# Optimization experiments

Hardware: AMD Instinct MI355X
Metric: run time of the kernel (lower is better)

The kernel has to match this reference:

```python
import jax, jax.numpy as jnp
import numpy as np

C = 256      # channel_num
K = 9        # key_num
B, H, W = 8, 64, 64


def setup_inputs() -> dict:
    key = jax.random.key(0)
    ks = jax.random.split(key, 12)
    s = 1.0 / np.sqrt(C)
    return {
        "query_layer": jax.random.normal(ks[0], (B, C, H, W), jnp.float32),
        "key_layer": jax.random.normal(ks[1], (B, C, H, W), jnp.float32),
        "gumbel_noise": jax.random.gumbel(ks[2], (B, K, H, W), jnp.float32),
        "w_refer": jax.random.normal(ks[3], (C, C), jnp.float32) * s,
        "b_refer": jax.random.normal(ks[4], (C,), jnp.float32) * 0.01,
        "w_attn": jax.random.normal(ks[5], (K, C), jnp.float32) * s,
        "b_attn": jax.random.normal(ks[6], (K,), jnp.float32) * 0.01,
        "w_mask": jax.random.normal(ks[7], (K, C), jnp.float32) * s,
        "b_mask": jax.random.normal(ks[8], (K,), jnp.float32) * 0.01,
        "w_off": jax.random.normal(ks[9], (2 * K, C), jnp.float32) * 0.02,
        "b_off": jax.random.normal(ks[10], (2 * K,), jnp.float32) * 0.01,
        "temp": 1,
    }


def _conv1x1(w, b, x):
    # w: (O,C), x: (B,C,H,W) -> (B,O,H,W)
    return jnp.einsum('oc,bchw->bohw', w, x) + b[None, :, None, None]


def _sample_one(img, py, px):
    # img: (C,H,W); py,px: (K,H,W) absolute sampling coords (bilinear, zero pad)
    h, w = img.shape[1], img.shape[2]
    y0 = jnp.floor(py)
    x0 = jnp.floor(px)
    wy = py - y0          # weight toward y0+1
    wx = px - x0

    def gather(yi, xi):
        valid = (yi >= 0) & (yi < h) & (xi >= 0) & (xi < w)
        yc = jnp.clip(yi, 0, h - 1).astype(jnp.int32)
        xc = jnp.clip(xi, 0, w - 1).astype(jnp.int32)
        return img[:, yc, xc] * valid[None].astype(img.dtype)  # (C,K,H,W)

    out = (gather(y0, x0) * ((1 - wy) * (1 - wx))[None]
           + gather(y0, x0 + 1) * ((1 - wy) * wx)[None]
           + gather(y0 + 1, x0) * (wy * (1 - wx))[None]
           + gather(y0 + 1, x0 + 1) * (wy * wx)[None])
    return out  # (C,K,H,W)


def reference(query_layer, key_layer, gumbel_noise, w_refer, b_refer,
              w_attn, b_attn, w_mask, b_mask, w_off, b_off, temp):
    key_feature = _conv1x1(w_refer, b_refer, key_layer)          # (B,C,H,W)
    attn_weights = _conv1x1(w_attn, b_attn, query_layer)         # (B,K,H,W)
    soft_mask = _conv1x1(w_mask, b_mask, query_layer)            # (B,K,H,W)
    # gumbel_softmax(hard=False) over key dim
    hard_mask = jax.nn.softmax((soft_mask + gumbel_noise) / temp, axis=1)
    offset = _conv1x1(w_off, b_off, query_layer)                 # (B,2K,H,W)

    # faithful to offset[:, i:i+2]: overlapping (dy,dx) slices
    dy = offset[:, 0:K]        # (B,K,H,W)
    dx = offset[:, 1:K + 1]    # (B,K,H,W)
    ys = jnp.arange(H, dtype=offset.dtype)[None, None, :, None]
    xs = jnp.arange(W, dtype=offset.dtype)[None, None, None, :]
    py = ys + dy
    px = xs + dx

    sampled = jax.vmap(_sample_one)(key_feature, py, px)         # (B,C,K,H,W)

    aw = jax.nn.softmax(attn_weights * hard_mask, axis=1)        # (B,K,H,W)
    out = jnp.einsum('bkhw,bckhw->bchw', aw, sampled)            # (B,C,H,W)
    return out
```

## Files before the change

### kernel.cpp

```cpp
#include <hip/hip_runtime.h>

typedef unsigned short u16;
typedef __attribute__((ext_vector_type(8))) short bf16x8;
typedef __attribute__((ext_vector_type(4))) float f32x4;

__device__ __forceinline__ u16 f2bf(float f) {
    unsigned u = __float_as_uint(f);
    unsigned r = (u + 0x7fffu + ((u >> 16) & 1u)) >> 16;
    return (u16)r;
}
__device__ __forceinline__ float bf2f(u16 h) {
    union { unsigned u; float f; } x; x.u = ((unsigned)h) << 16; return x.f;
}

#define NB 8
#define NC 256
#define NK 9
#define NH 64
#define NW 64
#define NP 4096
#define BAND 320
#define SB_STRIDE 328
#define KS_STRIDE 264

__global__ __launch_bounds__(256) void kf_gemm(const float* __restrict__ key,
                                               const float* __restrict__ w_refer,
                                               const float* __restrict__ b_refer,
                                               u16* __restrict__ kf16)
{
    __shared__ u16 K_s[64 * KS_STRIDE];
    const int bid = blockIdx.x;
    const int b   = bid >> 6;
    const int p0  = (bid & 63) << 6;
    const int t = threadIdx.x;
    const int lane = t & 63, wid = t >> 6;
    const int fr = lane & 15, kq = (lane >> 4) << 3;
    const int co0w = wid << 6;

    #pragma unroll
    for (int rep = 0; rep < 16; ++rep) {
        int k = (rep << 4) + (t >> 4), px4 = (t & 15) << 2;
        float4 v = *(const float4*)&key[((size_t)b * NC + k) * NP + p0 + px4];
        K_s[(px4 + 0) * KS_STRIDE + k] = f2bf(v.x);
        K_s[(px4 + 1) * KS_STRIDE + k] = f2bf(v.y);
        K_s[(px4 + 2) * KS_STRIDE + k] = f2bf(v.z);
        K_s[(px4 + 3) * KS_STRIDE + k] = f2bf(v.w);
    }
    __syncthreads();

    f32x4 acc[4][4];
    #pragma unroll
    for (int i = 0; i < 4; ++i)
        #pragma unroll
        for (int j = 0; j < 4; ++j) acc[i][j] = (f32x4){0.f, 0.f, 0.f, 0.f};

    for (int ks = 0; ks < 8; ++ks) {
        const int k0 = (ks << 5) + kq;
        bf16x8 af[4], bfv[4];
        #pragma unroll
        for (int mi = 0; mi < 4; ++mi) {
            const float* src = &w_refer[(size_t)(co0w + (mi << 4) + fr) * NC + k0];
            float4 v0 = *(const float4*)src;
            float4 v1 = *(const float4*)(src + 4);
            bf16x8 a;
            a[0] = (short)f2bf(v0.x); a[1] = (short)f2bf(v0.y);
            a[2] = (short)f2bf(v0.z); a[3] = (short)f2bf(v0.w);
            a[4] = (short)f2bf(v1.x); a[5] = (short)f2bf(v1.y);
            a[6] = (short)f2bf(v1.z); a[7] = (short)f2bf(v1.w);
            af[mi] = a;
        }
        #pragma unroll
        for (int ni = 0; ni < 4; ++ni)
            bfv[ni] = *(const bf16x8*)&K_s[((ni << 4) + fr) * KS_STRIDE + k0];
        #pragma unroll
        for (int mi = 0; mi < 4; ++mi)
            #pragma unroll
            for (int ni = 0; ni < 4; ++ni)
                acc[mi][ni] = __builtin_amdgcn_mfma_f32_16x16x32_bf16(af[mi], bfv[ni], acc[mi][ni], 0, 0, 0);
    }
    const int col = lane & 15, rbase = (lane >> 4) << 2;
    #pragma unroll
    for (int mi = 0; mi < 4; ++mi) {
        #pragma unroll
        for (int rr = 0; rr < 4; ++rr) {
            int co = co0w + (mi << 4) + rbase + rr;
            float bias = b_refer[co];
            u16* dst = &kf16[((size_t)b * NC + co) * NP + p0 + col];
            #pragma unroll
            for (int ni = 0; ni < 4; ++ni)
                dst[ni << 4] = f2bf(acc[mi][ni][rr] + bias);
        }
    }
}

__global__ __launch_bounds__(256) void head_meta(const float* __restrict__ query,
                                                 const float* __restrict__ gumbel,
                                                 const float* __restrict__ w_attn, const float* __restrict__ b_attn,
                                                 const float* __restrict__ w_mask, const float* __restrict__ b_mask,
                                                 const float* __restrict__ w_off,  const float* __restrict__ b_off,
                                                 const int* __restrict__ temp_p,
                                                 float4* __restrict__ wgt, uint2* __restrict__ offs)
{
    __shared__ u16 A[48][264];
    __shared__ float hdT[128][41];
    const int pt = blockIdx.x;
    const int b  = pt >> 5;
    const int p0 = (pt & 31) << 7;
    const int t = threadIdx.x;
    const int lane = t & 63, wn = t >> 6;
    const int fr = lane & 15, kq = (lane >> 4) << 3;

    for (int i = t; i < 1152; i += 256) {
        int o = i >> 5, c = (i & 31) << 3;
        const float* src = (o < 9) ? &w_attn[o * NC + c]
                       : (o < 18 ? &w_mask[(o - 9) * NC + c]
                                 : &w_off[(o - 18) * NC + c]);
        float4 v0 = *(const float4*)src;
        float4 v1 = *(const float4*)(src + 4);
        bf16x8 a;
        a[0] = (short)f2bf(v0.x); a[1] = (short)f2bf(v0.y);
        a[2] = (short)f2bf(v0.z); a[3] = (short)f2bf(v0.w);
        a[4] = (short)f2bf(v1.x); a[5] = (short)f2bf(v1.y);
        a[6] = (short)f2bf(v1.z); a[7] = (short)f2bf(v1.w);
        *(bf16x8*)&A[o][c] = a;
    }
    for (int i = t; i < 384; i += 256) {
        bf16x8 z = {0,0,0,0,0,0,0,0};
        *(bf16x8*)&A[36 + (i >> 5)][(i & 31) << 3] = z;
    }
    __syncthreads();

    f32x4 acc[3][2];
    #pragma unroll
    for (int i = 0; i < 3; ++i)
        #pragma unroll
        for (int j = 0; j < 2; ++j) acc[i][j] = (f32x4){0.f, 0.f, 0.f, 0.f};

    for (int ks = 0; ks < 8; ++ks) {
        const int k0 = (ks << 5) + kq;
        bf16x8 af[3], bfv[2];
        #pragma unroll
        for (int mi = 0; mi < 3; ++mi)
            af[mi] = *(const bf16x8*)&A[(mi << 4) + fr][k0];
        #pragma unroll
        for (int ni = 0; ni < 2; ++ni) {
            const float* src = &query[((size_t)b * NC + k0) * NP + p0 + (wn << 5) + (ni << 4) + fr];
            bf16x8 bv;
            #pragma unroll
            for (int j = 0; j < 8; ++j) bv[j] = (short)f2bf(src[(size_t)j * NP]);
            bfv[ni] = bv;
        }
        #pragma unroll
        for (int mi = 0; mi < 3; ++mi)
            #pragma unroll
            for (int ni = 0; ni < 2; ++ni)
                acc[mi][ni] = __builtin_amdgcn_mfma_f32_16x16x32_bf16(af[mi], bfv[ni], acc[mi][ni], 0, 0, 0);
    }
    const int col = lane & 15, rbase = (lane >> 4) << 2;
    #pragma unroll
    for (int mi = 0; mi < 3; ++mi) {
        #pragma unroll
        for (int rr = 0; rr < 4; ++rr) {
            int o = (mi << 4) + rbase + rr;
            if (o < 36) {
                float bias = (o < 9) ? b_attn[o] : (o < 18) ? b_mask[o - 9] : b_off[o - 18];
                #pragma unroll
                for (int ni = 0; ni < 2; ++ni)
                    hdT[(wn << 5) + (ni << 4) + col][o] = acc[mi][ni][rr] + bias;
            }
        }
    }
    __syncthreads();

    if (t < 128) {
        const int pxg = p0 + t;
        const int row = pxg >> 6, xcol = pxg & 63;
        float v[36];
        #pragma unroll
        for (int o = 0; o < 36; ++o) v[o] = hdT[t][o];

        int ti = temp_p[0];
        float tempf = (ti >= 1 && ti < (1 << 23)) ? (float)ti : __int_as_float(ti);
        float am[9], hs[9];
        float mx = -1e30f;
        #pragma unroll
        for (int k = 0; k < 9; ++k) {
            am[k] = v[k];
            float g = gumbel[((size_t)b * NK + k) * NP + pxg];
            hs[k] = (v[9 + k] + g) / tempf;
            mx = fmaxf(mx, hs[k]);
        }
        float ssum = 0.f;
        #pragma unroll
        for (int k = 0; k < 9; ++k) { hs[k] = __expf(hs[k] - mx); ssum += hs[k]; }
        float inv = 1.f / ssum;
        float lg[9]; float mx2 = -1e30f;
        #pragma unroll
        for (int k = 0; k < 9; ++k) { lg[k] = am[k] * (hs[k] * inv); mx2 = fmaxf(mx2, lg[k]); }
        float s2 = 0.f;
        #pragma unroll
        for (int k = 0; k < 9; ++k) { lg[k] = __expf(lg[k] - mx2); s2 += lg[k]; }
        float inv2 = 1.f / s2;
        #pragma unroll
        for (int k = 0; k < 9; ++k) {
            float a = lg[k] * inv2;
            float pyv = (float)row  + v[18 + k];
            float pxv = (float)xcol + v[19 + k];
            float y0f = floorf(pyv), x0f = floorf(pxv);
            float wy = pyv - y0f, wx = pxv - x0f;
            int y0 = (int)y0f, x0 = (int)x0f;
            int y1 = y0 + 1, x1 = x0 + 1;
            float vy0 = (y0 >= 0 && y0 < NH) ? 1.f : 0.f;
            float vy1 = (y1 >= 0 && y1 < NH) ? 1.f : 0.f;
            float vx0 = (x0 >= 0 && x0 < NW) ? 1.f : 0.f;
            float vx1 = (x1 >= 0 && x1 < NW) ? 1.f : 0.f;
            int y0c = min(max(y0, 0), NH - 1), y1c = min(max(y1, 0), NH - 1);
            int x0c = min(max(x0, 0), NW - 1), x1c = min(max(x1, 0), NW - 1);
            unsigned o00 = (unsigned)(y0c * NW + x0c), o01 = (unsigned)(y0c * NW + x1c);
            unsigned o10 = (unsigned)(y1c * NW + x0c), o11 = (unsigned)(y1c * NW + x1c);
            size_t idx = ((size_t)b * NK + k) * NP + pxg;
            wgt[idx]  = make_float4(a * (1.f - wy) * (1.f - wx) * vy0 * vx0,
                                    a * (1.f - wy) * wx * vy0 * vx1,
                                    a * wy * (1.f - wx) * vy1 * vx0,
                                    a * wy * wx * vy1 * vx1);
            offs[idx] = make_uint2(o00 | (o01 << 16), o10 | (o11 << 16));
        }
    }
}

__global__ __launch_bounds__(512, 4) void sample_pass(const u16* __restrict__ kf16,
                                                      const float4* __restrict__ wgt,
                                                      const uint2* __restrict__ offs,
                                                      float* __restrict__ out)
{
    __shared__ float Sf[64][BAND];

    const int bid = blockIdx.x;
    const int b = bid & 7, row = bid >> 3;
    const int t = threadIdx.x;
    const int lane = t & 63, wid = t >> 6;
    const int fr = lane & 15, kq = (lane >> 4) << 3;
    const int c0 = wid << 5;
    const int ylo = min(max(row - 2, 0), NH - 5);
    const int base = ylo << 6;
    const u16* kfb = kf16 + (size_t)b * NC * NP + base;

    const int px = t & 63, kg = t >> 6;
    size_t idx0 = ((size_t)b * NK + kg) * NP + (row << 6) + px;
    float4 wv0 = wgt[idx0];
    uint2  ov0 = offs[idx0];
    float4 wv1 = make_float4(0.f, 0.f, 0.f, 0.f);
    uint2  ov1 = make_uint2(0u, 0u);
    if (kg == 0) {
        size_t idx1 = ((size_t)b * NK + 8) * NP + (row << 6) + px;
        wv1 = wgt[idx1]; ov1 = offs[idx1];
    }

    #pragma unroll
    for (int i = 0; i < 10; ++i)
        ((float4*)Sf)[t + (i << 9)] = (float4){0.f, 0.f, 0.f, 0.f};
    __syncthreads();

    bool esc = false;
    #pragma unroll
    for (int s = 0; s < 2; ++s) {
        if (s == 1 && kg != 0) break;
        float4 wv = s ? wv1 : wv0;
        uint2  ov = s ? ov1 : ov0;
        int   o4[4] = { (int)(ov.x & 0xffffu), (int)(ov.x >> 16),
                        (int)(ov.y & 0xffffu), (int)(ov.y >> 16) };
        float w4[4] = { wv.x, wv.y, wv.z, wv.w };
        #pragma unroll
        for (int c = 0; c < 4; ++c) {
            int u = o4[c] - base;
            if ((unsigned)u < (unsigned)BAND) atomicAdd(&Sf[px][u], w4[c]);
            else esc = true;
        }
    }
    __syncthreads();

    bf16x8 apre[4][2];
    #pragma unroll
    for (int s = 0; s < 4; ++s)
        #pragma unroll
        for (int mi = 0; mi < 2; ++mi)
            apre[s][mi] = *(const bf16x8*)&kfb[(size_t)(c0 + (mi << 4) + fr) * NP + (s << 5) + kq];

    u16* Sb = (u16*)&Sf[0][0];
    #pragma unroll
    for (int r = 0; r < 5; ++r) {
        int i = t + (r << 9);
        int p = i / 40, j = (i % 40) << 3;
        float4 a = *(const float4*)&Sf[p][j];
        float4 c = *(const float4*)&Sf[p][j + 4];
        bf16x8 q;
        q[0] = (short)f2bf(a.x); q[1] = (short)f2bf(a.y);
        q[2] = (short)f2bf(a.z); q[3] = (short)f2bf(a.w);
        q[4] = (short)f2bf(c.x); q[5] = (short)f2bf(c.y);
        q[6] = (short)f2bf(c.z); q[7] = (short)f2bf(c.w);
        __syncthreads();
        *(bf16x8*)&Sb[p * SB_STRIDE + j] = q;
    }
    __syncthreads();

    f32x4 acc[2][4];
    #pragma unroll
    for (int i = 0; i < 2; ++i)
        #pragma unroll
        for (int j = 0; j < 4; ++j) acc[i][j] = (f32x4){0.f, 0.f, 0.f, 0.f};

    #pragma unroll
    for (int step = 0; step < 10; ++step) {
        bf16x8 a0 = apre[step & 3][0], a1 = apre[step & 3][1];
        if (step + 4 < 10) {
            #pragma unroll
            for (int mi = 0; mi < 2; ++mi)
                apre[step & 3][mi] =
                    *(const bf16x8*)&kfb[(size_t)(c0 + (mi << 4) + fr) * NP + ((step + 4) << 5) + kq];
        }
        bf16x8 bfv[4];
        #pragma unroll
        for (int ni = 0; ni < 4; ++ni)
            bfv[ni] = *(const bf16x8*)&Sb[((ni << 4) + fr) * SB_STRIDE + (step << 5) + kq];
        #pragma unroll
        for (int ni = 0; ni < 4; ++ni) {
            acc[0][ni] = __builtin_amdgcn_mfma_f32_16x16x32_bf16(a0, bfv[ni], acc[0][ni], 0, 0, 0);
            acc[1][ni] = __builtin_amdgcn_mfma_f32_16x16x32_bf16(a1, bfv[ni], acc[1][ni], 0, 0, 0);
        }
    }

    const int col = lane & 15, rbase = (lane >> 4) << 2;
    float* ob = out + (size_t)b * NC * NP + (row << 6);
    #pragma unroll
    for (int mi = 0; mi < 2; ++mi) {
        #pragma unroll
        for (int rr = 0; rr < 4; ++rr) {
            int c = c0 + (mi << 4) + rbase + rr;
            #pragma unroll
            for (int ni = 0; ni < 4; ++ni)
                ob[(size_t)c * NP + (ni << 4) + col] = acc[mi][ni][rr];
        }
    }

    __syncthreads();
    if (esc) {
        for (int s = 0; s < (kg == 0 ? 2 : 1); ++s) {
            int k = s ? 8 : kg;
            size_t idx = ((size_t)b * NK + k) * NP + (row << 6) + px;
            float4 wv = wgt[idx];
            uint2  ov = offs[idx];
            int   o4[4] = { (int)(ov.x & 0xffffu), (int)(ov.x >> 16),
                            (int)(ov.y & 0xffffu), (int)(ov.y >> 16) };
            float w4[4] = { wv.x, wv.y, wv.z, wv.w };
            for (int c = 0; c < 4; ++c) {
                int u = o4[c] - base;
                if ((unsigned)u >= (unsigned)BAND) {
                    for (int cc = 0; cc < NC; ++cc)
                        atomicAdd(&ob[(size_t)cc * NP + px],
                                  w4[c] * bf2f(kf16[((size_t)b * NC + cc) * NP + o4[c]]));
                }
            }
        }
    }
}

extern "C" void kernel_launch(void* const* d_in, const int* in_sizes, int n_in,
                              void* d_out, int out_size, void* d_ws, size_t ws_size,
                              hipStream_t stream)
{
    const float* query   = (const float*)d_in[0];
    const float* key     = (const float*)d_in[1];
    const float* gumbel  = (const float*)d_in[2];
    const float* w_refer = (const float*)d_in[3];
    const float* b_refer = (const float*)d_in[4];
    const float* w_attn  = (const float*)d_in[5];
    const float* b_attn  = (const float*)d_in[6];
    const float* w_mask  = (const float*)d_in[7];
    const float* b_mask  = (const float*)d_in[8];
    const float* w_off   = (const float*)d_in[9];
    const float* b_off   = (const float*)d_in[10];
    const int*   temp    = (const int*)d_in[11];
    float* out = (float*)d_out;

    u16*    kf16 = (u16*)d_ws;
    float4* wgt  = (float4*)((char*)d_ws + (size_t)NB * NP * NC * 2);
    uint2*  offs = (uint2*)((char*)wgt + (size_t)NB * NK * NP * 16);

    kf_gemm<<<512, 256, 0, stream>>>(key, w_refer, b_refer, kf16);
    head_meta<<<256, 256, 0, stream>>>(query, gumbel, w_attn, b_attn, w_mask, b_mask,
                                       w_off, b_off, temp, wgt, offs);
    sample_pass<<<512, 512, 0, stream>>>(kf16, wgt, offs, out);
}
```

Before: 62.10 us.

## Merge kf_gemm and head_meta into one launch; batch sample_pass LDS syncs

Fuses the key-feature GEMM and the head/metadata kernel into a single 768-block launch. Blocks are split by index and share one union shared-memory buffer, and the batch index is now interleaved across blocks. This removes a launch boundary and lets the two independent producers run concurrently on the GPU. In sample_pass, the kf prefetch is hoisted above the scatter phase so its loads overlap the atomics, and the five per-iteration __syncthreads in the bf16 repack are collapsed to one by buffering packed values in registers. The trade-offs are higher register pressure and a larger shared-memory footprint for the gemm blocks.

```diff
diff --git a/kernel.cpp b/kernel.cpp
--- a/kernel.cpp
+++ b/kernel.cpp
@@ -23,43 +23,97 @@
 #define SB_STRIDE 328
 #define KS_STRIDE 264
 
-__global__ __launch_bounds__(256) void kf_gemm(const float* __restrict__ key,
-                                               const float* __restrict__ w_refer,
-                                               const float* __restrict__ b_refer,
-                                               u16* __restrict__ kf16)
+__global__ __launch_bounds__(256) void prep(const float* __restrict__ key,
+                                            const float* __restrict__ query,
+                                            const float* __restrict__ gumbel,
+                                            const float* __restrict__ w_refer,
+                                            const float* __restrict__ b_refer,
+                                            const float* __restrict__ w_attn, const float* __restrict__ b_attn,
+                                            const float* __restrict__ w_mask, const float* __restrict__ b_mask,
+                                            const float* __restrict__ w_off,  const float* __restrict__ b_off,
+                                            const int* __restrict__ temp_p,
+                                            u16* __restrict__ kf16,
+                                            float4* __restrict__ wgt, uint2* __restrict__ offs)
 {
-    __shared__ u16 K_s[64 * KS_STRIDE];
-    const int bid = blockIdx.x;
-    const int b   = bid >> 6;
-    const int p0  = (bid & 63) << 6;
+    __shared__ __align__(16) char smem[46336];
     const int t = threadIdx.x;
     const int lane = t & 63, wid = t >> 6;
     const int fr = lane & 15, kq = (lane >> 4) << 3;
-    const int co0w = wid << 6;
-
-    #pragma unroll
-    for (int rep = 0; rep < 16; ++rep) {
-        int k = (rep << 4) + (t >> 4), px4 = (t & 15) << 2;
-        float4 v = *(const float4*)&key[((size_t)b * NC + k) * NP + p0 + px4];
-        K_s[(px4 + 0) * KS_STRIDE + k] = f2bf(v.x);
-        K_s[(px4 + 1) * KS_STRIDE + k] = f2bf(v.y);
-        K_s[(px4 + 2) * KS_STRIDE + k] = f2bf(v.z);
-        K_s[(px4 + 3) * KS_STRIDE + k] = f2bf(v.w);
-    }
-    __syncthreads();
-
-    f32x4 acc[4][4];
-    #pragma unroll
-    for (int i = 0; i < 4; ++i)
-        #pragma unroll
-        for (int j = 0; j < 4; ++j) acc[i][j] = (f32x4){0.f, 0.f, 0.f, 0.f};
-
-    for (int ks = 0; ks < 8; ++ks) {
-        const int k0 = (ks << 5) + kq;
-        bf16x8 af[4], bfv[4];
+
+    if (blockIdx.x < 512) {
+        u16* K_s = (u16*)smem;
+        const int bid = blockIdx.x;
+        const int b   = bid & 7;
+        const int p0  = (bid >> 3) << 6;
+        const int co0w = wid << 6;
+
+        #pragma unroll
+        for (int rep = 0; rep < 16; ++rep) {
+            int k = (rep << 4) + (t >> 4), px4 = (t & 15) << 2;
+            float4 v = *(const float4*)&key[((size_t)b * NC + k) * NP + p0 + px4];
+            K_s[(px4 + 0) * KS_STRIDE + k] = f2bf(v.x);
+            K_s[(px4 + 1) * KS_STRIDE + k] = f2bf(v.y);
+            K_s[(px4 + 2) * KS_STRIDE + k] = f2bf(v.z);
+            K_s[(px4 + 3) * KS_STRIDE + k] = f2bf(v.w);
+        }
+        __syncthreads();
+
+        f32x4 acc[4][4];
+        #pragma unroll
+        for (int i = 0; i < 4; ++i)
+            #pragma unroll
+            for (int j = 0; j < 4; ++j) acc[i][j] = (f32x4){0.f, 0.f, 0.f, 0.f};
+
+        for (int ks = 0; ks < 8; ++ks) {
+            const int k0 = (ks << 5) + kq;
+            bf16x8 af[4], bfv[4];
+            #pragma unroll
+            for (int mi = 0; mi < 4; ++mi) {
+                const float* src = &w_refer[(size_t)(co0w + (mi << 4) + fr) * NC + k0];
+                float4 v0 = *(const float4*)src;
+                float4 v1 = *(const float4*)(src + 4);
+                bf16x8 a;
+                a[0] = (short)f2bf(v0.x); a[1] = (short)f2bf(v0.y);
+                a[2] = (short)f2bf(v0.z); a[3] = (short)f2bf(v0.w);
+                a[4] = (short)f2bf(v1.x); a[5] = (short)f2bf(v1.y);
+                a[6] = (short)f2bf(v1.z); a[7] = (short)f2bf(v1.w);
+                af[mi] = a;
+            }
+            #pragma unroll
+            for (int ni = 0; ni < 4; ++ni)
+                bfv[ni] = *(const bf16x8*)&K_s[((ni << 4) + fr) * KS_STRIDE + k0];
+            #pragma unroll
+            for (int mi = 0; mi < 4; ++mi)
+                #pragma unroll
+                for (int ni = 0; ni < 4; ++ni)
+                    acc[mi][ni] = __builtin_amdgcn_mfma_f32_16x16x32_bf16(af[mi], bfv[ni], acc[mi][ni], 0, 0, 0);
+        }
+        const int col = lane & 15, rbase = (lane >> 4) << 2;
         #pragma unroll
         for (int mi = 0; mi < 4; ++mi) {
-            const float* src = &w_refer[(size_t)(co0w + (mi << 4) + fr) * NC + k0];
+            #pragma unroll
+            for (int rr = 0; rr < 4; ++rr) {
+                int co = co0w + (mi << 4) + rbase + rr;
+                float bias = b_refer[co];
+                u16* dst = &kf16[((size_t)b * NC + co) * NP + p0 + col];
+                #pragma unroll
+                for (int ni = 0; ni < 4; ++ni)
+                    dst[ni << 4] = f2bf(acc[mi][ni][rr] + bias);
+            }
+        }
+    } else {
+        const int pt = (int)blockIdx.x - 512;
+        const int b  = pt & 7;
+        const int p0 = (pt >> 3) << 7;
+        u16   (*A)[264] = (u16(*)[264])smem;
+        float (*hdT)[41] = (float(*)[41])(smem + 25344);
+        const int wn = wid;
+
+        for (int i = t; i < 1152; i += 256) {
+            int o = i >> 5, c = (i & 31) << 3;
+            const float* src = (o < 9) ? &w_attn[o * NC + c]
+                           : (o < 18 ? &w_mask[(o - 9) * NC + c]
+                                     : &w_off[(o - 18) * NC + c]);
             float4 v0 = *(const float4*)src;
             float4 v1 = *(const float4*)(src + 4);
             bf16x8 a;
@@ -67,163 +121,109 @@
             a[2] = (short)f2bf(v0.z); a[3] = (short)f2bf(v0.w);
             a[4] = (short)f2bf(v1.x); a[5] = (short)f2bf(v1.y);
             a[6] = (short)f2bf(v1.z); a[7] = (short)f2bf(v1.w);
-            af[mi] = a;
-        }
-        #pragma unroll
-        for (int ni = 0; ni < 4; ++ni)
-            bfv[ni] = *(const bf16x8*)&K_s[((ni << 4) + fr) * KS_STRIDE + k0];
-        #pragma unroll
-        for (int mi = 0; mi < 4; ++mi)
-            #pragma unroll
-            for (int ni = 0; ni < 4; ++ni)
-                acc[mi][ni] = __builtin_amdgcn_mfma_f32_16x16x32_bf16(af[mi], bfv[ni], acc[mi][ni], 0, 0, 0);
-    }
-    const int col = lane & 15, rbase = (lane >> 4) << 2;
-    #pragma unroll
-    for (int mi = 0; mi < 4; ++mi) {
-        #pragma unroll
-        for (int rr = 0; rr < 4; ++rr) {
-            int co = co0w + (mi << 4) + rbase + rr;
-            float bias = b_refer[co];
-            u16* dst = &kf16[((size_t)b * NC + co) * NP + p0 + col];
-            #pragma unroll
-            for (int ni = 0; ni < 4; ++ni)
-                dst[ni << 4] = f2bf(acc[mi][ni][rr] + bias);
-        }
-    }
-}
-
-__global__ __launch_bounds__(256) void head_meta(const float* __restrict__ query,
-                                                 const float* __restrict__ gumbel,
-                                                 const float* __restrict__ w_attn, const float* __restrict__ b_attn,
-                                                 const float* __restrict__ w_mask, const float* __restrict__ b_mask,
-                                                 const float* __restrict__ w_off,  const float* __restrict__ b_off,
-                                                 const int* __restrict__ temp_p,
-                                                 float4* __restrict__ wgt, uint2* __restrict__ offs)
-{
-    __shared__ u16 A[48][264];
-    __shared__ float hdT[128][41];
-    const int pt = blockIdx.x;
-    const int b  = pt >> 5;
-    const int p0 = (pt & 31) << 7;
-    const int t = threadIdx.x;
-    const int lane = t & 63, wn = t >> 6;
-    const int fr = lane & 15, kq = (lane >> 4) << 3;
-
-    for (int i = t; i < 1152; i += 256) {
-        int o = i >> 5, c = (i & 31) << 3;
-        const float* src = (o < 9) ? &w_attn[o * NC + c]
-                       : (o < 18 ? &w_mask[(o - 9) * NC + c]
-                                 : &w_off[(o - 18) * NC + c]);
-        float4 v0 = *(const float4*)src;
-        float4 v1 = *(const float4*)(src + 4);
-        bf16x8 a;
-        a[0] = (short)f2bf(v0.x); a[1] = (short)f2bf(v0.y);
-        a[2] = (short)f2bf(v0.z); a[3] = (short)f2bf(v0.w);
-        a[4] = (short)f2bf(v1.x); a[5] = (short)f2bf(v1.y);
-        a[6] = (short)f2bf(v1.z); a[7] = (short)f2bf(v1.w);
-        *(bf16x8*)&A[o][c] = a;
-    }
-    for (int i = t; i < 384; i += 256) {
-        bf16x8 z = {0,0,0,0,0,0,0,0};
-        *(bf16x8*)&A[36 + (i >> 5)][(i & 31) << 3] = z;
-    }
-    __syncthreads();
-
-    f32x4 acc[3][2];
-    #pragma unroll
-    for (int i = 0; i < 3; ++i)
-        #pragma unroll
-        for (int j = 0; j < 2; ++j) acc[i][j] = (f32x4){0.f, 0.f, 0.f, 0.f};
-
-    for (int ks = 0; ks < 8; ++ks) {
-        const int k0 = (ks << 5) + kq;
-        bf16x8 af[3], bfv[2];
-        #pragma unroll
-        for (int mi = 0; mi < 3; ++mi)
-            af[mi] = *(const bf16x8*)&A[(mi << 4) + fr][k0];
-        #pragma unroll
-        for (int ni = 0; ni < 2; ++ni) {
-            const float* src = &query[((size_t)b * NC + k0) * NP + p0 + (wn << 5) + (ni << 4) + fr];
-            bf16x8 bv;
-            #pragma unroll
-            for (int j = 0; j < 8; ++j) bv[j] = (short)f2bf(src[(size_t)j * NP]);
-            bfv[ni] = bv;
-        }
-        #pragma unroll
-        for (int mi = 0; mi < 3; ++mi)
-            #pragma unroll
-            for (int ni = 0; ni < 2; ++ni)
-                acc[mi][ni] = __builtin_amdgcn_mfma_f32_16x16x32_bf16(af[mi], bfv[ni], acc[mi][ni], 0, 0, 0);
-    }
-    const int col = lane & 15, rbase = (lane >> 4) << 2;
-    #pragma unroll
-    for (int mi = 0; mi < 3; ++mi) {
-        #pragma unroll
-        for (int rr = 0; rr < 4; ++rr) {
-            int o = (mi << 4) + rbase + rr;
-            if (o < 36) {
-                float bias = (o < 9) ? b_attn[o] : (o < 18) ? b_mask[o - 9] : b_off[o - 18];
+            *(bf16x8*)&A[o][c] = a;
+        }
+        for (int i = t; i < 384; i += 256) {
+            bf16x8 z = {0,0,0,0,0,0,0,0};
+            *(bf16x8*)&A[36 + (i >> 5)][(i & 31) << 3] = z;
+        }
+        __syncthreads();
+
+        f32x4 acc[3][2];
+        #pragma unroll
+        for (int i = 0; i < 3; ++i)
+            #pragma unroll
+            for (int j = 0; j < 2; ++j) acc[i][j] = (f32x4){0.f, 0.f, 0.f, 0.f};
+
+        for (int ks = 0; ks < 8; ++ks) {
+            const int k0 = (ks << 5) + kq;
+            bf16x8 af[3], bfv[2];
+            #pragma unroll
+            for (int mi = 0; mi < 3; ++mi)
+                af[mi] = *(const bf16x8*)&A[(mi << 4) + fr][k0];
+            #pragma unroll
+            for (int ni = 0; ni < 2; ++ni) {
+                const float* src = &query[((size_t)b * NC + k0) * NP + p0 + (wn << 5) + (ni << 4) + fr];
+                bf16x8 bv;
+                #pragma unroll
+                for (int j = 0; j < 8; ++j) bv[j] = (short)f2bf(src[(size_t)j * NP]);
+                bfv[ni] = bv;
+            }
+            #pragma unroll
+            for (int mi = 0; mi < 3; ++mi)
                 #pragma unroll
                 for (int ni = 0; ni < 2; ++ni)
-                    hdT[(wn << 5) + (ni << 4) + col][o] = acc[mi][ni][rr] + bias;
-            }
-        }
-    }
-    __syncthreads();
-
-    if (t < 128) {
-        const int pxg = p0 + t;
-        const int row = pxg >> 6, xcol = pxg & 63;
-        float v[36];
-        #pragma unroll
-        for (int o = 0; o < 36; ++o) v[o] = hdT[t][o];
-
-        int ti = temp_p[0];
-        float tempf = (ti >= 1 && ti < (1 << 23)) ? (float)ti : __int_as_float(ti);
-        float am[9], hs[9];
-        float mx = -1e30f;
-        #pragma unroll
-        for (int k = 0; k < 9; ++k) {
-            am[k] = v[k];
-            float g = gumbel[((size_t)b * NK + k) * NP + pxg];
-            hs[k] = (v[9 + k] + g) / tempf;
-            mx = fmaxf(mx, hs[k]);
-        }
-        float ssum = 0.f;
-        #pragma unroll
-        for (int k = 0; k < 9; ++k) { hs[k] = __expf(hs[k] - mx); ssum += hs[k]; }
-        float inv = 1.f / ssum;
-        float lg[9]; float mx2 = -1e30f;
-        #pragma unroll
-        for (int k = 0; k < 9; ++k) { lg[k] = am[k] * (hs[k] * inv); mx2 = fmaxf(mx2, lg[k]); }
-        float s2 = 0.f;
-        #pragma unroll
-        for (int k = 0; k < 9; ++k) { lg[k] = __expf(lg[k] - mx2); s2 += lg[k]; }
-        float inv2 = 1.f / s2;
-        #pragma unroll
-        for (int k = 0; k < 9; ++k) {
-            float a = lg[k] * inv2;
-            float pyv = (float)row  + v[18 + k];
-            float pxv = (float)xcol + v[19 + k];
-            float y0f = floorf(pyv), x0f = floorf(pxv);
-            float wy = pyv - y0f, wx = pxv - x0f;
-            int y0 = (int)y0f, x0 = (int)x0f;
-            int y1 = y0 + 1, x1 = x0 + 1;
-            float vy0 = (y0 >= 0 && y0 < NH) ? 1.f : 0.f;
-            float vy1 = (y1 >= 0 && y1 < NH) ? 1.f : 0.f;
-            float vx0 = (x0 >= 0 && x0 < NW) ? 1.f : 0.f;
-            float vx1 = (x1 >= 0 && x1 < NW) ? 1.f : 0.f;
-            int y0c = min(max(y0, 0), NH - 1), y1c = min(max(y1, 0), NH - 1);
-            int x0c = min(max(x0, 0), NW - 1), x1c = min(max(x1, 0), NW - 1);
-            unsigned o00 = (unsigned)(y0c * NW + x0c), o01 = (unsigned)(y0c * NW + x1c);
-            unsigned o10 = (unsigned)(y1c * NW + x0c), o11 = (unsigned)(y1c * NW + x1c);
-            size_t idx = ((size_t)b * NK + k) * NP + pxg;
-            wgt[idx]  = make_float4(a * (1.f - wy) * (1.f - wx) * vy0 * vx0,
-                                    a * (1.f - wy) * wx * vy0 * vx1,
-                                    a * wy * (1.f - wx) * vy1 * vx0,
-                                    a * wy * wx * vy1 * vx1);
-            offs[idx] = make_uint2(o00 | (o01 << 16), o10 | (o11 << 16));
+                    acc[mi][ni] = __builtin_amdgcn_mfma_f32_16x16x32_bf16(af[mi], bfv[ni], acc[mi][ni], 0, 0, 0);
+        }
+        const int col = lane & 15, rbase = (lane >> 4) << 2;
+        #pragma unroll
+        for (int mi = 0; mi < 3; ++mi) {
+            #pragma unroll
+            for (int rr = 0; rr < 4; ++rr) {
+                int o = (mi << 4) + rbase + rr;
+                if (o < 36) {
+                    float bias = (o < 9) ? b_attn[o] : (o < 18) ? b_mask[o - 9] : b_off[o - 18];
+                    #pragma unroll
+                    for (int ni = 0; ni < 2; ++ni)
+                        hdT[(wn << 5) + (ni << 4) + col][o] = acc[mi][ni][rr] + bias;
+                }
+            }
+        }
+        __syncthreads();
+
+        if (t < 128) {
+            const int pxg = p0 + t;
+            const int row = pxg >> 6, xcol = pxg & 63;
+            float v[36];
+            #pragma unroll
+            for (int o = 0; o < 36; ++o) v[o] = hdT[t][o];
+
+            int ti = temp_p[0];
+            float tempf = (ti >= 1 && ti < (1 << 23)) ? (float)ti : __int_as_float(ti);
+            float am[9], hs[9];
+            float mx = -1e30f;
+            #pragma unroll
+            for (int k = 0; k < 9; ++k) {
+                am[k] = v[k];
+                float g = gumbel[((size_t)b * NK + k) * NP + pxg];
+                hs[k] = (v[9 + k] + g) / tempf;
+                mx = fmaxf(mx, hs[k]);
+            }
+            float ssum = 0.f;
+            #pragma unroll
+            for (int k = 0; k < 9; ++k) { hs[k] = __expf(hs[k] - mx); ssum += hs[k]; }
+            float inv = 1.f / ssum;
+            float lg[9]; float mx2 = -1e30f;
+            #pragma unroll
+            for (int k = 0; k < 9; ++k) { lg[k] = am[k] * (hs[k] * inv); mx2 = fmaxf(mx2, lg[k]); }
+            float s2 = 0.f;
+            #pragma unroll
+            for (int k = 0; k < 9; ++k) { lg[k] = __expf(lg[k] - mx2); s2 += lg[k]; }
+            float inv2 = 1.f / s2;
+            #pragma unroll
+            for (int k = 0; k < 9; ++k) {
+                float a = lg[k] * inv2;
+                float pyv = (float)row  + v[18 + k];
+                float pxv = (float)xcol + v[19 + k];
+                float y0f = floorf(pyv), x0f = floorf(pxv);
+                float wy = pyv - y0f, wx = pxv - x0f;
+                int y0 = (int)y0f, x0 = (int)x0f;
+                int y1 = y0 + 1, x1 = x0 + 1;
+                float vy0 = (y0 >= 0 && y0 < NH) ? 1.f : 0.f;
+                float vy1 = (y1 >= 0 && y1 < NH) ? 1.f : 0.f;
+                float vx0 = (x0 >= 0 && x0 < NW) ? 1.f : 0.f;
+                float vx1 = (x1 >= 0 && x1 < NW) ? 1.f : 0.f;
+                int y0c = min(max(y0, 0), NH - 1), y1c = min(max(y1, 0), NH - 1);
+                int x0c = min(max(x0, 0), NW - 1), x1c = min(max(x1, 0), NW - 1);
+                unsigned o00 = (unsigned)(y0c * NW + x0c), o01 = (unsigned)(y0c * NW + x1c);
+                unsigned o10 = (unsigned)(y1c * NW + x0c), o11 = (unsigned)(y1c * NW + x1c);
+                size_t idx = ((size_t)b * NK + k) * NP + pxg;
+                wgt[idx]  = make_float4(a * (1.f - wy) * (1.f - wx) * vy0 * vx0,
+                                        a * (1.f - wy) * wx * vy0 * vx1,
+                                        a * wy * (1.f - wx) * vy1 * vx0,
+                                        a * wy * wx * vy1 * vx1);
+                offs[idx] = make_uint2(o00 | (o01 << 16), o10 | (o11 << 16));
+            }
         }
     }
 }
@@ -245,6 +245,13 @@
     const int base = ylo << 6;
     const u16* kfb = kf16 + (size_t)b * NC * NP + base;
 
+    bf16x8 apre[4][2];
+    #pragma unroll
+    for (int s = 0; s < 4; ++s)
+        #pragma unroll
+        for (int mi = 0; mi < 2; ++mi)
+            apre[s][mi] = *(const bf16x8*)&kfb[(size_t)(c0 + (mi << 4) + fr) * NP + (s << 5) + kq];
+
     const int px = t & 63, kg = t >> 6;
     size_t idx0 = ((size_t)b * NK + kg) * NP + (row << 6) + px;
     float4 wv0 = wgt[idx0];
@@ -279,14 +286,8 @@
     }
     __syncthreads();
 
-    bf16x8 apre[4][2];
-    #pragma unroll
-    for (int s = 0; s < 4; ++s)
-        #pragma unroll
-        for (int mi = 0; mi < 2; ++mi)
-            apre[s][mi] = *(const bf16x8*)&kfb[(size_t)(c0 + (mi << 4) + fr) * NP + (s << 5) + kq];
-
     u16* Sb = (u16*)&Sf[0][0];
+    bf16x8 pk[5]; int po[5];
     #pragma unroll
     for (int r = 0; r < 5; ++r) {
         int i = t + (r << 9);
@@ -298,9 +299,12 @@
         q[2] = (short)f2bf(a.z); q[3] = (short)f2bf(a.w);
         q[4] = (short)f2bf(c.x); q[5] = (short)f2bf(c.y);
         q[6] = (short)f2bf(c.z); q[7] = (short)f2bf(c.w);
-        __syncthreads();
-        *(bf16x8*)&Sb[p * SB_STRIDE + j] = q;
-    }
+        pk[r] = q; po[r] = p * SB_STRIDE + j;
+    }
+    __syncthreads();
+    #pragma unroll
+    for (int r = 0; r < 5; ++r)
+        *(bf16x8*)&Sb[po[r]] = pk[r];
     __syncthreads();
 
     f32x4 acc[2][4];
@@ -386,8 +390,8 @@
     float4* wgt  = (float4*)((char*)d_ws + (size_t)NB * NP * NC * 2);
     uint2*  offs = (uint2*)((char*)wgt + (size_t)NB * NK * NP * 16);
 
-    kf_gemm<<<512, 256, 0, stream>>>(key, w_refer, b_refer, kf16);
-    head_meta<<<256, 256, 0, stream>>>(query, gumbel, w_attn, b_attn, w_mask, b_mask,
-                                       w_off, b_off, temp, wgt, offs);
+    prep<<<768, 256, 0, stream>>>(key, query, gumbel, w_refer, b_refer,
+                                  w_attn, b_attn, w_mask, b_mask, w_off, b_off,
+                                  temp, kf16, wgt, offs);
     sample_pass<<<512, 512, 0, stream>>>(kf16, wgt, offs, out);
 }
```

New measurement: 65.89 us. 6.1% more time.
